# Performance work log

Measured on AMD Instinct MI355X. Metric: run time of the kernel, lower is better.

The kernel has to match this reference:

```python
import jax, jax.numpy as jnp
import numpy as np

E, EDIM, NDIM, H = 262144, 256, 256, 8
DH = NDIM // H
EPS = 1e-5  # torch nn.LayerNorm default


def _param(k, shape, scale=0.02):
    return jax.random.normal(k, shape, jnp.float32) * scale


def setup_inputs() -> dict:
    key = jax.random.key(0)
    ks = jax.random.split(key, 12)
    return {
        "x": jax.random.normal(ks[0], (E, EDIM), jnp.float32),
        "src_x": jax.random.normal(ks[1], (E, NDIM), jnp.float32),
        "dst_x": jax.random.normal(ks[2], (E, NDIM), jnp.float32),
        # multi-head cross-attention params (q from edge feats, k/v from node feats)
        "Wq": _param(ks[3], (EDIM, NDIM)), "bq": jnp.zeros((NDIM,), jnp.float32),
        "Wk": _param(ks[4], (NDIM, NDIM)), "bk": jnp.zeros((NDIM,), jnp.float32),
        "Wv": _param(ks[5], (NDIM, NDIM)), "bv": jnp.zeros((NDIM,), jnp.float32),
        "Wo": _param(ks[6], (NDIM, EDIM)), "bo": jnp.zeros((EDIM,), jnp.float32),
        "W1": _param(ks[7], (EDIM, 4 * EDIM)), "b1": jnp.zeros((4 * EDIM,), jnp.float32),
        "W2": _param(ks[8], (4 * EDIM, EDIM)), "b2": jnp.zeros((EDIM,), jnp.float32),
        # two LayerNorms
        "g1": jnp.ones((EDIM,), jnp.float32), "be1": jnp.zeros((EDIM,), jnp.float32),
        "g2": jnp.ones((EDIM,), jnp.float32), "be2": jnp.zeros((EDIM,), jnp.float32),
    }


def _layer_norm(h, g, b):
    m = jnp.mean(h, axis=-1, keepdims=True)
    v = jnp.mean(jnp.square(h - m), axis=-1, keepdims=True)
    return (h - m) * jax.lax.rsqrt(v + EPS) * g + b


def reference(x, src_x, dst_x, Wq, bq, Wk, bk, Wv, bv, Wo, bo,
              W1, b1, W2, b2, g1, be1, g2, be2):
    # per-edge cross-attention: query = edge feat (len 1), keys/values = (src, dst) (len 2)
    q = (x @ Wq + bq).reshape(E, H, DH)                 # [E,H,DH]
    kv = jnp.stack([src_x, dst_x], axis=1)              # [E,2,NDIM]
    k = (kv @ Wk + bk).reshape(E, 2, H, DH)
    v = (kv @ Wv + bv).reshape(E, 2, H, DH)
    scale = 1.0 / float(np.sqrt(DH))
    scores = jnp.einsum('ehd,ekhd->ehk', q, k) * scale  # [E,H,2]
    attn = jax.nn.softmax(scores, axis=-1)
    ctx = jnp.einsum('ehk,ekhd->ehd', attn, v).reshape(E, NDIM)
    out = ctx @ Wo + bo                                  # [E,EDIM]
    h = _layer_norm(x + out, g1, be1)
    ff = jax.nn.relu(h @ W1 + b1) @ W2 + b2
    return _layer_norm(h + ff, g2, be2)
```

## Files before the change

### kernel.cpp

```cpp
#include <hip/hip_runtime.h>
#include <hip/hip_bf16.h>
#include <math.h>

#define NROWS   262144
#define BM      64
#define THREADS 256
#define LDSB_A  (32768 + 32768 + 2048 + 512)
#define LDSB_B  (32768 + 16384 + 2048 + 512)

using bf16x8 = __attribute__((ext_vector_type(8))) short;
using s16x4  = __attribute__((ext_vector_type(4))) short;
using f32x4  = __attribute__((ext_vector_type(4))) float;

__device__ __forceinline__ short f2bf(float f) {
  __hip_bfloat16 h = __float2bfloat16(f);
  return __builtin_bit_cast(short, h);
}
__device__ __forceinline__ float bf2f(short s) {
  __hip_bfloat16 h = __builtin_bit_cast(__hip_bfloat16, s);
  return __bfloat162float(h);
}
__device__ __forceinline__ unsigned pack2(float a, float b) {
  return (unsigned)(unsigned short)f2bf(a) | ((unsigned)(unsigned short)f2bf(b) << 16);
}
template <int RSTR>
__device__ __forceinline__ int swzR(int row, int col) {
  return row * RSTR + ((col * 2) ^ ((row & 7) << 4));
}
__device__ __forceinline__ int swz(int row, int col) {
  return swzR<512>(row, col);
}

__device__ __forceinline__ float red16(float p) {
  p += __shfl_xor(p, 1, 64);
  p += __shfl_xor(p, 2, 64);
  p += __shfl_xor(p, 4, 64);
  p += __shfl_xor(p, 8, 64);
  return p;
}

template <int MF, int NF, int KLEN = 256, int RSTR = 512>
__device__ __forceinline__ void gemmT(const char* __restrict__ Abuf,
                                      const short* __restrict__ WT, int Kw,
                                      int col0, int koff, int li, int hi,
                                      f32x4 (&acc)[MF][NF]) {
  const short* wp[NF];
#pragma unroll
  for (int n = 0; n < NF; ++n)
    wp[n] = WT + (size_t)(col0 + 16 * n + li) * Kw + koff + hi * 8;
#pragma unroll 2
  for (int kk = 0; kk < KLEN; kk += 32) {
    int ka = kk + hi * 8;
    bf16x8 b[NF];
#pragma unroll
    for (int n = 0; n < NF; ++n) b[n] = *(const bf16x8*)(wp[n] + kk);
    bf16x8 a[MF];
#pragma unroll
    for (int m = 0; m < MF; ++m)
      a[m] = *(const bf16x8*)(Abuf + swzR<RSTR>(16 * m + li, ka));
#pragma unroll
    for (int m = 0; m < MF; ++m)
#pragma unroll
      for (int n = 0; n < NF; ++n)
        acc[m][n] = __builtin_amdgcn_mfma_f32_16x16x32_bf16(a[m], b[n], acc[m][n], 0, 0, 0);
  }
}

__global__ void prep(const float* __restrict__ Wq, const float* __restrict__ Wk,
                     const float* __restrict__ Wv, const float* __restrict__ Wo,
                     const float* __restrict__ W1, const float* __restrict__ W2,
                     short* __restrict__ wt) {
  int idx = blockIdx.x * blockDim.x + threadIdx.x;
  if (idx < 262144) {
    int m = idx >> 16;
    const float* W = (m == 0) ? Wq : (m == 1) ? Wk : (m == 2) ? Wv : Wo;
    float s = (m == 0) ? 0.17677669529663687f : 1.0f;
    int l = idx & 65535;
    int n = l >> 8, k = l & 255;
    wt[idx] = f2bf(W[k * 256 + n] * s);
  } else if (idx < 524288) {
    int l = idx - 262144;
    int n = l >> 8, k = l & 255;
    wt[idx] = f2bf(W1[k * 1024 + n]);
  } else {
    int l = idx - 524288;
    int n = l >> 10, k = l & 1023;
    wt[idx] = f2bf(W2[k * 256 + n]);
  }
}

__global__ __launch_bounds__(THREADS, 2)
void attn_ln1(const float* __restrict__ x, const float* __restrict__ sx,
              const float* __restrict__ dx,
              const float* __restrict__ bq, const float* __restrict__ bv,
              const float* __restrict__ bo,
              const float* __restrict__ g1, const float* __restrict__ be1,
              const short* __restrict__ wt, short* __restrict__ hout) {
  extern __shared__ char sm[];
  char*  Cbuf = sm;
  char*  Tbuf = sm + 32768;
  float* sc   = (float*)(sm + 65536);
  float* scrM = (float*)(sm + 67584);

  const short* WqT = wt;
  const short* WkT = wt + 65536;
  const short* WvT = wt + 131072;
  const short* WoT = wt + 196608;

  const int tid  = threadIdx.x;
  const int w    = tid >> 6;
  const int lane = tid & 63;
  const int li   = lane & 15;
  const int hi   = lane >> 4;
  const int cw   = w * 64;
  const size_t row0 = (size_t)blockIdx.x * BM;

  const float* xt = x  + row0 * 256;
  const float* st = sx + row0 * 256;
  const float* dt = dx + row0 * 256;

  float4 ld[16];

#pragma unroll
  for (int it = 0; it < 16; ++it) {
    int idx = it * THREADS + tid;
    ld[it] = *(const float4*)(xt + (idx >> 6) * 256 + ((idx & 63) << 2));
  }
#pragma unroll
  for (int it = 0; it < 16; ++it) {
    int idx = it * THREADS + tid;
    int r = idx >> 6, c = (idx & 63) << 2;
    s16x4 o;
    o[0] = f2bf(ld[it].x); o[1] = f2bf(ld[it].y);
    o[2] = f2bf(ld[it].z); o[3] = f2bf(ld[it].w);
    *(s16x4*)(Cbuf + swz(r, c)) = o;
  }
  __syncthreads();

#pragma unroll
  for (int it = 0; it < 16; ++it) {
    int idx = it * THREADS + tid;
    ld[it] = *(const float4*)(dt + (idx >> 6) * 256 + ((idx & 63) << 2));
  }
  unsigned qb[4][4][2];
  {
    f32x4 qa[4][4];
#pragma unroll
    for (int m = 0; m < 4; ++m)
#pragma unroll
      for (int n = 0; n < 4; ++n) qa[m][n] = (f32x4){0.f, 0.f, 0.f, 0.f};
    gemmT<4, 4>(Cbuf, WqT, 256, cw, 0, li, hi, qa);
    const float scl = 0.17677669529663687f;
#pragma unroll
    for (int n = 0; n < 4; ++n) {
      float bqn = bq[cw + 16 * n + li] * scl;
#pragma unroll
      for (int m = 0; m < 4; ++m) {
        qb[m][n][0] = pack2(qa[m][n][0] + bqn, qa[m][n][1] + bqn);
        qb[m][n][1] = pack2(qa[m][n][2] + bqn, qa[m][n][3] + bqn);
      }
    }
  }
#pragma unroll
  for (int it = 0; it < 16; ++it) {
    int idx = it * THREADS + tid;
    int r = idx >> 6, c = (idx & 63) << 2;
    s16x4 o;
    o[0] = f2bf(ld[it].x); o[1] = f2bf(ld[it].y);
    o[2] = f2bf(ld[it].z); o[3] = f2bf(ld[it].w);
    *(s16x4*)(Tbuf + swz(r, c)) = o;
  }
  __syncthreads();

#define QF(m, n, j) bf2f((short)(((j) & 1) ? (qb[m][n][(j) >> 1] >> 16) \
                                           : (qb[m][n][(j) >> 1] & 0xffffu)))

#pragma unroll
  for (int it = 0; it < 16; ++it) {
    int idx = it * THREADS + tid;
    ld[it] = *(const float4*)(st + (idx >> 6) * 256 + ((idx & 63) << 2));
  }
#pragma unroll
  for (int hh = 0; hh < 2; ++hh) {
    f32x4 ka[4][2];
#pragma unroll
    for (int m = 0; m < 4; ++m)
#pragma unroll
      for (int n = 0; n < 2; ++n) ka[m][n] = (f32x4){0.f, 0.f, 0.f, 0.f};
    gemmT<4, 2>(Tbuf, WkT, 256, cw + 32 * hh, 0, li, hi, ka);
#pragma unroll
    for (int m = 0; m < 4; ++m)
#pragma unroll
      for (int j = 0; j < 4; ++j) {
        float pr = red16(QF(m, 2 * hh, j) * ka[m][0][j] +
                         QF(m, 2 * hh + 1, j) * ka[m][1][j]);
        if (li == 0) sc[(w * 2 + hh) * 64 + 16 * m + 4 * hi + j] = pr;
      }
  }
  f32x4 vd[4][4];
#pragma unroll
  for (int m = 0; m < 4; ++m)
#pragma unroll
    for (int n = 0; n < 4; ++n) vd[m][n] = (f32x4){0.f, 0.f, 0.f, 0.f};
  gemmT<4, 4>(Tbuf, WvT, 256, cw, 0, li, hi, vd);
  __syncthreads();
#pragma unroll
  for (int it = 0; it < 16; ++it) {
    int idx = it * THREADS + tid;
    int r = idx >> 6, c = (idx & 63) << 2;
    s16x4 o;
    o[0] = f2bf(ld[it].x); o[1] = f2bf(ld[it].y);
    o[2] = f2bf(ld[it].z); o[3] = f2bf(ld[it].w);
    *(s16x4*)(Tbuf + swz(r, c)) = o;
  }
  __syncthreads();

#pragma unroll
  for (int hh = 0; hh < 2; ++hh) {
    f32x4 ka[4][2];
#pragma unroll
    for (int m = 0; m < 4; ++m)
#pragma unroll
      for (int n = 0; n < 2; ++n) ka[m][n] = (f32x4){0.f, 0.f, 0.f, 0.f};
    gemmT<4, 2>(Tbuf, WkT, 256, cw + 32 * hh, 0, li, hi, ka);
#pragma unroll
    for (int m = 0; m < 4; ++m)
#pragma unroll
      for (int j = 0; j < 4; ++j) {
        float ps = red16(QF(m, 2 * hh, j) * ka[m][0][j] +
                         QF(m, 2 * hh + 1, j) * ka[m][1][j]);
        int r = 16 * m + 4 * hi + j;
        float pdv = sc[(w * 2 + hh) * 64 + r];
        float awv = 1.f / (1.f + expf(pdv - ps));
        if (li == 0) sc[(w * 2 + hh) * 64 + r] = awv;
      }
  }
  {
    f32x4 vs[4][4];
#pragma unroll
    for (int m = 0; m < 4; ++m)
#pragma unroll
      for (int n = 0; n < 4; ++n) vs[m][n] = (f32x4){0.f, 0.f, 0.f, 0.f};
    gemmT<4, 4>(Tbuf, WvT, 256, cw, 0, li, hi, vs);
#pragma unroll
    for (int hh = 0; hh < 2; ++hh)
#pragma unroll
      for (int n2 = 0; n2 < 2; ++n2) {
        int n = 2 * hh + n2;
        float bvn = bv[cw + 16 * n + li];
#pragma unroll
        for (int m = 0; m < 4; ++m)
#pragma unroll
          for (int j = 0; j < 4; ++j) {
            float a = sc[(w * 2 + hh) * 64 + 16 * m + 4 * hi + j];
            vs[m][n][j] = a * vs[m][n][j] + (1.f - a) * vd[m][n][j] + bvn;
          }
      }
    __syncthreads();
#pragma unroll
    for (int m = 0; m < 4; ++m)
#pragma unroll
      for (int n = 0; n < 4; ++n)
#pragma unroll
        for (int j = 0; j < 4; ++j)
          *(short*)(Tbuf + swz(16 * m + 4 * hi + j, cw + 16 * n + li)) = f2bf(vs[m][n][j]);
  }
  __syncthreads();

  {
    f32x4 oa[4][4];
#pragma unroll
    for (int m = 0; m < 4; ++m)
#pragma unroll
      for (int n = 0; n < 4; ++n) oa[m][n] = (f32x4){0.f, 0.f, 0.f, 0.f};
    gemmT<4, 4>(Tbuf, WoT, 256, cw, 0, li, hi, oa);
#pragma unroll
    for (int n = 0; n < 4; ++n) {
      float bon = bo[cw + 16 * n + li];
#pragma unroll
      for (int m = 0; m < 4; ++m)
#pragma unroll
        for (int j = 0; j < 4; ++j) {
          int r = 16 * m + 4 * hi + j;
          float xv = bf2f(*(short*)(Cbuf + swz(r, cw + 16 * n + li)));
          oa[m][n][j] += bon + xv;
        }
    }
#pragma unroll
    for (int m = 0; m < 4; ++m)
#pragma unroll
      for (int j = 0; j < 4; ++j) {
        int r = 16 * m + 4 * hi + j;
        float sv = oa[m][0][j] + oa[m][1][j] + oa[m][2][j] + oa[m][3][j];
        float qv = oa[m][0][j] * oa[m][0][j] + oa[m][1][j] * oa[m][1][j]
                 + oa[m][2][j] * oa[m][2][j] + oa[m][3][j] * oa[m][3][j];
        float s = red16(sv);
        float q = red16(qv);
        if (li == 0) { sc[(w * 64 + r) * 2] = s; sc[(w * 64 + r) * 2 + 1] = q; }
      }
    __syncthreads();
    if (tid < BM) {
      float S = 0.f, Q = 0.f;
#pragma unroll
      for (int ww = 0; ww < 4; ++ww) {
        S += sc[(ww * 64 + tid) * 2];
        Q += sc[(ww * 64 + tid) * 2 + 1];
      }
      float mean = S * (1.f / 256.f);
      float var  = Q * (1.f / 256.f) - mean * mean;
      scrM[tid * 2] = mean;
      scrM[tid * 2 + 1] = rsqrtf(var + 1e-5f);
    }
    __syncthreads();
#pragma unroll
    for (int n = 0; n < 4; ++n) {
      float g1n = g1[cw + 16 * n + li];
      float b1n = be1[cw + 16 * n + li];
#pragma unroll
      for (int m = 0; m < 4; ++m)
#pragma unroll
        for (int j = 0; j < 4; ++j) {
          int r = 16 * m + 4 * hi + j;
          float mean = scrM[r * 2], rs = scrM[r * 2 + 1];
          *(short*)(Cbuf + swz(r, cw + 16 * n + li)) =
              f2bf((oa[m][n][j] - mean) * rs * g1n + b1n);
        }
    }
  }
  __syncthreads();

  {
    short* hrow = hout + row0 * 256;
#pragma unroll
    for (int t = 0; t < 8; ++t) {
      int idx = t * THREADS + tid;
      int r = idx >> 5, c16 = idx & 31;
      bf16x8 v = *(bf16x8*)(Cbuf + r * 512 + ((c16 * 16) ^ ((r & 7) << 4)));
      *(bf16x8*)(hrow + r * 256 + c16 * 8) = v;
    }
  }
#undef QF
}

__global__ __launch_bounds__(THREADS, 3)
void ffn_ln2(const short* __restrict__ hin, const float* __restrict__ b1,
             const float* __restrict__ b2,
             const float* __restrict__ g2, const float* __restrict__ be2,
             const short* __restrict__ wt, float* __restrict__ out) {
  extern __shared__ char sm[];
  char* Cbuf = sm;
  char* Hbuf = sm + 32768;
  float* scrC  = (float*)(sm + 49152);
  float* scr2C = (float*)(sm + 51200);

  const short* W1T = wt + 262144;
  const short* W2T = wt + 524288;

  const int tid  = threadIdx.x;
  const int w    = tid >> 6;
  const int lane = tid & 63;
  const int li   = lane & 15;
  const int hi   = lane >> 4;
  const int cw   = w * 64;
  const size_t row0 = (size_t)blockIdx.x * BM;

  {
    const short* hrow = hin + row0 * 256;
#pragma unroll
    for (int t = 0; t < 8; ++t) {
      int idx = t * THREADS + tid;
      int r = idx >> 5, c16 = idx & 31;
      bf16x8 v = *(const bf16x8*)(hrow + r * 256 + c16 * 8);
      *(bf16x8*)(Cbuf + r * 512 + ((c16 * 16) ^ ((r & 7) << 4))) = v;
    }
  }
  __syncthreads();

  f32x4 a2[4][4];
#pragma unroll
  for (int m = 0; m < 4; ++m)
#pragma unroll
    for (int n = 0; n < 4; ++n) a2[m][n] = (f32x4){0.f, 0.f, 0.f, 0.f};
#pragma unroll 1
  for (int c = 0; c < 8; ++c) {
#pragma unroll
    for (int f = 0; f < 2; ++f) {
      f32x4 a1[4][1];
#pragma unroll
      for (int m = 0; m < 4; ++m) a1[m][0] = (f32x4){0.f, 0.f, 0.f, 0.f};
      int col0 = 128 * c + 32 * w + 16 * f;
      gemmT<4, 1, 256, 512>(Cbuf, W1T, 256, col0, 0, li, hi, a1);
      float b1n = b1[col0 + li];
      int lc = 32 * w + 16 * f + li;
#pragma unroll
      for (int m = 0; m < 4; ++m)
#pragma unroll
        for (int j = 0; j < 4; ++j) {
          int r = 16 * m + 4 * hi + j;
          *(short*)(Hbuf + swzR<256>(r, lc)) = f2bf(fmaxf(a1[m][0][j] + b1n, 0.f));
        }
    }
    __syncthreads();
    gemmT<4, 4, 128, 256>(Hbuf, W2T, 1024, cw, 128 * c, li, hi, a2);
    __syncthreads();
  }

  {
#pragma unroll
    for (int n = 0; n < 4; ++n) {
      float b2n = b2[cw + 16 * n + li];
#pragma unroll
      for (int m = 0; m < 4; ++m)
#pragma unroll
        for (int j = 0; j < 4; ++j) {
          int r = 16 * m + 4 * hi + j;
          a2[m][n][j] += b2n + bf2f(*(short*)(Cbuf + swz(r, cw + 16 * n + li)));
        }
    }
  }
  __syncthreads();

#pragma unroll
  for (int m = 0; m < 4; ++m)
#pragma unroll
    for (int j = 0; j < 4; ++j) {
      int r = 16 * m + 4 * hi + j;
      float sv = a2[m][0][j] + a2[m][1][j] + a2[m][2][j] + a2[m][3][j];
      float qv = a2[m][0][j] * a2[m][0][j] + a2[m][1][j] * a2[m][1][j]
               + a2[m][2][j] * a2[m][2][j] + a2[m][3][j] * a2[m][3][j];
      float s = red16(sv);
      float q = red16(qv);
      if (li == 0) { scrC[(w * 64 + r) * 2] = s; scrC[(w * 64 + r) * 2 + 1] = q; }
    }
  __syncthreads();
  if (tid < BM) {
    float S = 0.f, Q = 0.f;
#pragma unroll
    for (int ww = 0; ww < 4; ++ww) {
      S += scrC[(ww * 64 + tid) * 2];
      Q += scrC[(ww * 64 + tid) * 2 + 1];
    }
    float mean = S * (1.f / 256.f);
    float var  = Q * (1.f / 256.f) - mean * mean;
    scr2C[tid * 2] = mean;
    scr2C[tid * 2 + 1] = rsqrtf(var + 1e-5f);
  }
  __syncthreads();

  {
    float g2n[4], b2n[4];
#pragma unroll
    for (int n = 0; n < 4; ++n) {
      g2n[n] = g2[cw + 16 * n + li];
      b2n[n] = be2[cw + 16 * n + li];
    }
    float* orow = out + row0 * 256;
#pragma unroll
    for (int hf = 0; hf < 2; ++hf) {
#pragma unroll
      for (int m2 = 0; m2 < 2; ++m2) {
        int m = 2 * hf + m2;
#pragma unroll
        for (int n = 0; n < 4; ++n)
#pragma unroll
          for (int j = 0; j < 4; ++j) {
            int r = 16 * m + 4 * hi + j;
            float mean = scr2C[r * 2], rs = scr2C[r * 2 + 1];
            int rr = r - 32 * hf;
            *(float*)(Cbuf + rr * 1024 + (((cw + 16 * n + li) * 4) ^ ((rr & 7) << 4)))
                = (a2[m][n][j] - mean) * rs * g2n[n] + b2n[n];
          }
      }
      __syncthreads();
#pragma unroll
      for (int t = 0; t < 8; ++t) {
        int idx = t * THREADS + tid;
        int r = idx >> 6, c4 = idx & 63;
        f32x4 v = *(f32x4*)(Cbuf + r * 1024 + ((c4 * 16) ^ ((r & 7) << 4)));
        *(f32x4*)(orow + (hf * 32 + r) * 256 + c4 * 4) = v;
      }
      __syncthreads();
    }
  }
}

extern "C" void kernel_launch(void* const* d_in, const int* in_sizes, int n_in,
                              void* d_out, int out_size, void* d_ws, size_t ws_size,
                              hipStream_t stream) {
  const float* x   = (const float*)d_in[0];
  const float* sx  = (const float*)d_in[1];
  const float* dx  = (const float*)d_in[2];
  const float* Wq  = (const float*)d_in[3];
  const float* bq  = (const float*)d_in[4];
  const float* Wk  = (const float*)d_in[5];
  const float* Wv  = (const float*)d_in[7];
  const float* bv  = (const float*)d_in[8];
  const float* Wo  = (const float*)d_in[9];
  const float* bo  = (const float*)d_in[10];
  const float* W1  = (const float*)d_in[11];
  const float* b1  = (const float*)d_in[12];
  const float* W2  = (const float*)d_in[13];
  const float* b2  = (const float*)d_in[14];
  const float* g1  = (const float*)d_in[15];
  const float* be1 = (const float*)d_in[16];
  const float* g2  = (const float*)d_in[17];
  const float* be2 = (const float*)d_in[18];
  short* wt = (short*)d_ws;
  short* hbuf = wt + 786432;

  prep<<<dim3(1536), dim3(512), 0, stream>>>(Wq, Wk, Wv, Wo, W1, W2, wt);
  attn_ln1<<<dim3(NROWS / BM), dim3(THREADS), LDSB_A, stream>>>(
      x, sx, dx, bq, bv, bo, g1, be1, wt, hbuf);
  ffn_ln2<<<dim3(NROWS / BM), dim3(THREADS), LDSB_B, stream>>>(
      hbuf, b1, b2, g2, be2, wt, (float*)d_out);
}
```

Measured before the change: 1.139 ms.

## Software-pipeline FFN chunks with double-buffered hidden tile and interleaved GEMMs

Restructures the FFN loop so the W1 GEMM for chunk c+1 is interleaved with the W2 GEMM for chunk c, writing the ReLU output into a double-buffered LDS hidden tile. This cuts one barrier per chunk and lets the MFMA work of the two GEMMs overlap each other's memory loads. LDS per block grows by 16 KB and the occupancy hint drops from 3 to 2 blocks per CU, which may reduce latency hiding. A prologue computes the first chunk and an epilogue finishes the last W2 chunk.

After: 1.127 ms. About the same (-1.0%).

```diff
diff --git a/kernel.cpp b/kernel.cpp
--- a/kernel.cpp
+++ b/kernel.cpp
@@ -6,7 +6,7 @@
 #define BM      64
 #define THREADS 256
 #define LDSB_A  (32768 + 32768 + 2048 + 512)
-#define LDSB_B  (32768 + 16384 + 2048 + 512)
+#define LDSB_B  (32768 + 32768 + 2048 + 512)
 
 using bf16x8 = __attribute__((ext_vector_type(8))) short;
 using s16x4  = __attribute__((ext_vector_type(4))) short;
@@ -63,6 +63,54 @@
 #pragma unroll
       for (int n = 0; n < NF; ++n)
         acc[m][n] = __builtin_amdgcn_mfma_f32_16x16x32_bf16(a[m], b[n], acc[m][n], 0, 0, 0);
+  }
+}
+
+__device__ __forceinline__ void ffn_phase(const char* __restrict__ Cbuf,
+                                          const char* __restrict__ Hcur,
+                                          const short* __restrict__ W1T, int w1col0,
+                                          const short* __restrict__ W2T, int w2koff,
+                                          int cw, int li, int hi,
+                                          f32x4 (&a1)[4][2], f32x4 (&a2)[4][4]) {
+  const short* w1p[2];
+#pragma unroll
+  for (int n = 0; n < 2; ++n)
+    w1p[n] = W1T + (size_t)(w1col0 + 16 * n + li) * 256 + hi * 8;
+  const short* w2p[4];
+#pragma unroll
+  for (int n = 0; n < 4; ++n)
+    w2p[n] = W2T + (size_t)(cw + 16 * n + li) * 1024 + w2koff + hi * 8;
+#pragma unroll
+  for (int s = 0; s < 8; ++s) {
+    int ka = 32 * s + hi * 8;
+    bf16x8 b1[2];
+    b1[0] = *(const bf16x8*)(w1p[0] + 32 * s);
+    b1[1] = *(const bf16x8*)(w1p[1] + 32 * s);
+    bf16x8 ax[4];
+#pragma unroll
+    for (int m = 0; m < 4; ++m)
+      ax[m] = *(const bf16x8*)(Cbuf + swzR<512>(16 * m + li, ka));
+#pragma unroll
+    for (int m = 0; m < 4; ++m) {
+      a1[m][0] = __builtin_amdgcn_mfma_f32_16x16x32_bf16(ax[m], b1[0], a1[m][0], 0, 0, 0);
+      a1[m][1] = __builtin_amdgcn_mfma_f32_16x16x32_bf16(ax[m], b1[1], a1[m][1], 0, 0, 0);
+    }
+    if ((s & 1) == 0) {
+      int kk = 16 * s;
+      int kh = kk + hi * 8;
+      bf16x8 b2[4];
+#pragma unroll
+      for (int n = 0; n < 4; ++n) b2[n] = *(const bf16x8*)(w2p[n] + kk);
+      bf16x8 ah[4];
+#pragma unroll
+      for (int m = 0; m < 4; ++m)
+        ah[m] = *(const bf16x8*)(Hcur + swzR<256>(16 * m + li, kh));
+#pragma unroll
+      for (int m = 0; m < 4; ++m)
+#pragma unroll
+        for (int n = 0; n < 4; ++n)
+          a2[m][n] = __builtin_amdgcn_mfma_f32_16x16x32_bf16(ah[m], b2[n], a2[m][n], 0, 0, 0);
+    }
   }
 }
 
@@ -342,16 +390,16 @@
 #undef QF
 }
 
-__global__ __launch_bounds__(THREADS, 3)
+__global__ __launch_bounds__(THREADS, 2)
 void ffn_ln2(const short* __restrict__ hin, const float* __restrict__ b1,
              const float* __restrict__ b2,
              const float* __restrict__ g2, const float* __restrict__ be2,
              const short* __restrict__ wt, float* __restrict__ out) {
   extern __shared__ char sm[];
   char* Cbuf = sm;
-  char* Hbuf = sm + 32768;
-  float* scrC  = (float*)(sm + 49152);
-  float* scr2C = (float*)(sm + 51200);
+  char* Hb   = sm + 32768;
+  float* scrC  = (float*)(sm + 65536);
+  float* scr2C = (float*)(sm + 67584);
 
   const short* W1T = wt + 262144;
   const short* W2T = wt + 524288;
@@ -376,34 +424,59 @@
   }
   __syncthreads();
 
+  {
+    f32x4 a1[4][2];
+#pragma unroll
+    for (int m = 0; m < 4; ++m)
+#pragma unroll
+      for (int n = 0; n < 2; ++n) a1[m][n] = (f32x4){0.f, 0.f, 0.f, 0.f};
+    gemmT<4, 2, 256, 512>(Cbuf, W1T, 256, 32 * w, 0, li, hi, a1);
+#pragma unroll
+    for (int n = 0; n < 2; ++n) {
+      float b1n = b1[32 * w + 16 * n + li];
+      int lc = 32 * w + 16 * n + li;
+#pragma unroll
+      for (int m = 0; m < 4; ++m)
+#pragma unroll
+        for (int j = 0; j < 4; ++j) {
+          int r = 16 * m + 4 * hi + j;
+          *(short*)(Hb + swzR<256>(r, lc)) = f2bf(fmaxf(a1[m][n][j] + b1n, 0.f));
+        }
+    }
+  }
+  __syncthreads();
+
   f32x4 a2[4][4];
 #pragma unroll
   for (int m = 0; m < 4; ++m)
 #pragma unroll
     for (int n = 0; n < 4; ++n) a2[m][n] = (f32x4){0.f, 0.f, 0.f, 0.f};
 #pragma unroll 1
-  for (int c = 0; c < 8; ++c) {
-#pragma unroll
-    for (int f = 0; f < 2; ++f) {
-      f32x4 a1[4][1];
-#pragma unroll
-      for (int m = 0; m < 4; ++m) a1[m][0] = (f32x4){0.f, 0.f, 0.f, 0.f};
-      int col0 = 128 * c + 32 * w + 16 * f;
-      gemmT<4, 1, 256, 512>(Cbuf, W1T, 256, col0, 0, li, hi, a1);
-      float b1n = b1[col0 + li];
-      int lc = 32 * w + 16 * f + li;
+  for (int c = 0; c < 7; ++c) {
+    const char* Hcur = Hb + (c & 1) * 16384;
+    char*       Hnxt = Hb + ((c + 1) & 1) * 16384;
+    f32x4 a1[4][2];
+#pragma unroll
+    for (int m = 0; m < 4; ++m)
+#pragma unroll
+      for (int n = 0; n < 2; ++n) a1[m][n] = (f32x4){0.f, 0.f, 0.f, 0.f};
+    ffn_phase(Cbuf, Hcur, W1T, 128 * (c + 1) + 32 * w, W2T, 128 * c,
+              cw, li, hi, a1, a2);
+#pragma unroll
+    for (int n = 0; n < 2; ++n) {
+      float b1n = b1[128 * (c + 1) + 32 * w + 16 * n + li];
+      int lc = 32 * w + 16 * n + li;
 #pragma unroll
       for (int m = 0; m < 4; ++m)
 #pragma unroll
         for (int j = 0; j < 4; ++j) {
           int r = 16 * m + 4 * hi + j;
-          *(short*)(Hbuf + swzR<256>(r, lc)) = f2bf(fmaxf(a1[m][0][j] + b1n, 0.f));
+          *(short*)(Hnxt + swzR<256>(r, lc)) = f2bf(fmaxf(a1[m][n][j] + b1n, 0.f));
         }
     }
     __syncthreads();
-    gemmT<4, 4, 128, 256>(Hbuf, W2T, 1024, cw, 128 * c, li, hi, a2);
-    __syncthreads();
-  }
+  }
+  gemmT<4, 4, 128, 256>(Hb + 16384, W2T, 1024, cw, 128 * 7, li, hi, a2);
 
   {
 #pragma unroll
```

## Run FFN kernel with 512 threads and 256-wide hidden chunks

Applied to the files above, without the earlier changes.

Doubles the FFN+LN2 block to 8 waves, so each wave owns 32 output columns instead of 64. The hidden dimension is now processed in 4 chunks of 256 instead of 8 chunks of 128, with a larger LDS hidden buffer. This halves the number of barrier-separated chunk iterations and cuts per-wave accumulator registers to raise parallelism. In exchange, LDS use per block grows, which may lower how many blocks fit per CU, and more waves reload the same weight tiles.

After: 1.170 ms. +2.8%, slower.

```diff
diff --git a/kernel.cpp b/kernel.cpp
--- a/kernel.cpp
+++ b/kernel.cpp
@@ -5,8 +5,9 @@
 #define NROWS   262144
 #define BM      64
 #define THREADS 256
+#define FTHREADS 512
 #define LDSB_A  (32768 + 32768 + 2048 + 512)
-#define LDSB_B  (32768 + 16384 + 2048 + 512)
+#define LDSB_B  (32768 + 32768 + 4096 + 512)
 
 using bf16x8 = __attribute__((ext_vector_type(8))) short;
 using s16x4  = __attribute__((ext_vector_type(4))) short;
@@ -342,7 +343,7 @@
 #undef QF
 }
 
-__global__ __launch_bounds__(THREADS, 3)
+__global__ __launch_bounds__(FTHREADS, 4)
 void ffn_ln2(const short* __restrict__ hin, const float* __restrict__ b1,
              const float* __restrict__ b2,
              const float* __restrict__ g2, const float* __restrict__ be2,
@@ -350,8 +351,8 @@
   extern __shared__ char sm[];
   char* Cbuf = sm;
   char* Hbuf = sm + 32768;
-  float* scrC  = (float*)(sm + 49152);
-  float* scr2C = (float*)(sm + 51200);
+  float* scrP = (float*)(sm + 65536);
+  float* scrM = (float*)(sm + 69632);
 
   const short* W1T = wt + 262144;
   const short* W2T = wt + 524288;
@@ -361,14 +362,14 @@
   const int lane = tid & 63;
   const int li   = lane & 15;
   const int hi   = lane >> 4;
-  const int cw   = w * 64;
+  const int cw   = w * 32;
   const size_t row0 = (size_t)blockIdx.x * BM;
 
   {
     const short* hrow = hin + row0 * 256;
 #pragma unroll
-    for (int t = 0; t < 8; ++t) {
-      int idx = t * THREADS + tid;
+    for (int t = 0; t < 4; ++t) {
+      int idx = t * FTHREADS + tid;
       int r = idx >> 5, c16 = idx & 31;
       bf16x8 v = *(const bf16x8*)(hrow + r * 256 + c16 * 8);
       *(bf16x8*)(Cbuf + r * 512 + ((c16 * 16) ^ ((r & 7) << 4))) = v;
@@ -376,38 +377,39 @@
   }
   __syncthreads();
 
-  f32x4 a2[4][4];
+  f32x4 a2[4][2];
 #pragma unroll
   for (int m = 0; m < 4; ++m)
 #pragma unroll
-    for (int n = 0; n < 4; ++n) a2[m][n] = (f32x4){0.f, 0.f, 0.f, 0.f};
+    for (int n = 0; n < 2; ++n) a2[m][n] = (f32x4){0.f, 0.f, 0.f, 0.f};
 #pragma unroll 1
-  for (int c = 0; c < 8; ++c) {
-#pragma unroll
-    for (int f = 0; f < 2; ++f) {
-      f32x4 a1[4][1];
-#pragma unroll
-      for (int m = 0; m < 4; ++m) a1[m][0] = (f32x4){0.f, 0.f, 0.f, 0.f};
-      int col0 = 128 * c + 32 * w + 16 * f;
-      gemmT<4, 1, 256, 512>(Cbuf, W1T, 256, col0, 0, li, hi, a1);
-      float b1n = b1[col0 + li];
-      int lc = 32 * w + 16 * f + li;
+  for (int c = 0; c < 4; ++c) {
+    f32x4 a1[4][2];
+#pragma unroll
+    for (int m = 0; m < 4; ++m)
+#pragma unroll
+      for (int n = 0; n < 2; ++n) a1[m][n] = (f32x4){0.f, 0.f, 0.f, 0.f};
+    gemmT<4, 2, 256, 512>(Cbuf, W1T, 256, 256 * c + cw, 0, li, hi, a1);
+#pragma unroll
+    for (int n = 0; n < 2; ++n) {
+      float b1n = b1[256 * c + cw + 16 * n + li];
+      int lc = cw + 16 * n + li;
 #pragma unroll
       for (int m = 0; m < 4; ++m)
 #pragma unroll
         for (int j = 0; j < 4; ++j) {
           int r = 16 * m + 4 * hi + j;
-          *(short*)(Hbuf + swzR<256>(r, lc)) = f2bf(fmaxf(a1[m][0][j] + b1n, 0.f));
+          *(short*)(Hbuf + swzR<512>(r, lc)) = f2bf(fmaxf(a1[m][n][j] + b1n, 0.f));
         }
     }
     __syncthreads();
-    gemmT<4, 4, 128, 256>(Hbuf, W2T, 1024, cw, 128 * c, li, hi, a2);
+    gemmT<4, 2, 256, 512>(Hbuf, W2T, 1024, cw, 256 * c, li, hi, a2);
     __syncthreads();
   }
 
   {
 #pragma unroll
-    for (int n = 0; n < 4; ++n) {
+    for (int n = 0; n < 2; ++n) {
       float b2n = b2[cw + 16 * n + li];
 #pragma unroll
       for (int m = 0; m < 4; ++m)
@@ -425,32 +427,31 @@
 #pragma unroll
     for (int j = 0; j < 4; ++j) {
       int r = 16 * m + 4 * hi + j;
-      float sv = a2[m][0][j] + a2[m][1][j] + a2[m][2][j] + a2[m][3][j];
-      float qv = a2[m][0][j] * a2[m][0][j] + a2[m][1][j] * a2[m][1][j]
-               + a2[m][2][j] * a2[m][2][j] + a2[m][3][j] * a2[m][3][j];
+      float sv = a2[m][0][j] + a2[m][1][j];
+      float qv = a2[m][0][j] * a2[m][0][j] + a2[m][1][j] * a2[m][1][j];
       float s = red16(sv);
       float q = red16(qv);
-      if (li == 0) { scrC[(w * 64 + r) * 2] = s; scrC[(w * 64 + r) * 2 + 1] = q; }
+      if (li == 0) { scrP[(w * 64 + r) * 2] = s; scrP[(w * 64 + r) * 2 + 1] = q; }
     }
   __syncthreads();
   if (tid < BM) {
     float S = 0.f, Q = 0.f;
 #pragma unroll
-    for (int ww = 0; ww < 4; ++ww) {
-      S += scrC[(ww * 64 + tid) * 2];
-      Q += scrC[(ww * 64 + tid) * 2 + 1];
+    for (int ww = 0; ww < 8; ++ww) {
+      S += scrP[(ww * 64 + tid) * 2];
+      Q += scrP[(ww * 64 + tid) * 2 + 1];
     }
     float mean = S * (1.f / 256.f);
     float var  = Q * (1.f / 256.f) - mean * mean;
-    scr2C[tid * 2] = mean;
-    scr2C[tid * 2 + 1] = rsqrtf(var + 1e-5f);
-  }
-  __syncthreads();
-
-  {
-    float g2n[4], b2n[4];
-#pragma unroll
-    for (int n = 0; n < 4; ++n) {
+    scrM[tid * 2] = mean;
+    scrM[tid * 2 + 1] = rsqrtf(var + 1e-5f);
+  }
+  __syncthreads();
+
+  {
+    float g2n[2], b2n[2];
+#pragma unroll
+    for (int n = 0; n < 2; ++n) {
       g2n[n] = g2[cw + 16 * n + li];
       b2n[n] = be2[cw + 16 * n + li];
     }
@@ -461,11 +462,11 @@
       for (int m2 = 0; m2 < 2; ++m2) {
         int m = 2 * hf + m2;
 #pragma unroll
-        for (int n = 0; n < 4; ++n)
+        for (int n = 0; n < 2; ++n)
 #pragma unroll
           for (int j = 0; j < 4; ++j) {
             int r = 16 * m + 4 * hi + j;
-            float mean = scr2C[r * 2], rs = scr2C[r * 2 + 1];
+            float mean = scrM[r * 2], rs = scrM[r * 2 + 1];
             int rr = r - 32 * hf;
             *(float*)(Cbuf + rr * 1024 + (((cw + 16 * n + li) * 4) ^ ((rr & 7) << 4)))
                 = (a2[m][n][j] - mean) * rs * g2n[n] + b2n[n];
@@ -473,8 +474,8 @@
       }
       __syncthreads();
 #pragma unroll
-      for (int t = 0; t < 8; ++t) {
-        int idx = t * THREADS + tid;
+      for (int t = 0; t < 4; ++t) {
+        int idx = t * FTHREADS + tid;
         int r = idx >> 6, c4 = idx & 63;
         f32x4 v = *(f32x4*)(Cbuf + r * 1024 + ((c4 * 16) ^ ((r & 7) << 4)));
         *(f32x4*)(orow + (hf * 32 + r) * 256 + c4 * 4) = v;
@@ -511,6 +512,6 @@
   prep<<<dim3(1536), dim3(512), 0, stream>>>(Wq, Wk, Wv, Wo, W1, W2, wt);
   attn_ln1<<<dim3(NROWS / BM), dim3(THREADS), LDSB_A, stream>>>(
       x, sx, dx, bq, bv, bo, g1, be1, wt, hbuf);
-  ffn_ln2<<<dim3(NROWS / BM), dim3(THREADS), LDSB_B, stream>>>(
+  ffn_ln2<<<dim3(NROWS / BM), dim3(FTHREADS), LDSB_B, stream>>>(
       hbuf, b1, b2, g2, be2, wt, (float*)d_out);
 }
```
